# Optimization experiments

Hardware: AMD Instinct MI355X
Metric: run time of the kernel (lower is better)

Reference implementation:

```python
import jax, jax.numpy as jnp
import numpy as np

# Module hyperparameters (from init_kwargs defaults)
SEQ_LEN = 250
MASK_RATIO = 0.6
NUM_SPANS = 3
SPAN_LEN = max(1, int(SEQ_LEN * MASK_RATIO / NUM_SPANS))  # 50
QRS_RADIUS = 30
CENTER = SEQ_LEN // 2  # 125
QRS_START = CENTER - QRS_RADIUS  # 95
QRS_END = CENTER + QRS_RADIUS    # 155
AVOID_PROB = 0.8
MAX_ATTEMPTS = 15


def setup_inputs() -> dict:
    key = jax.random.key(0)
    x = jax.random.normal(key, (16384, 12, SEQ_LEN), dtype=jnp.float32)
    return {"x": x}


def _span_starts(key, B):
    """Vectorized replacement for the host-side rejection-sampling loop.

    For each (batch, span): decide QRS avoidance, draw MAX_ATTEMPTS candidate
    starts at once, take the first valid one, fall back to a fresh draw if all
    attempts overlap the QRS zone (same semantics as the torch retry loop).
    """
    k1, k2, k3 = jax.random.split(key, 3)
    hi = max(1, SEQ_LEN - SPAN_LEN)  # exclusive upper bound = 200
    use_physio = jax.random.uniform(k1, (B, NUM_SPANS)) < AVOID_PROB
    cands = jax.random.randint(k2, (B, NUM_SPANS, MAX_ATTEMPTS), 0, hi)  # (B,S,A)
    ends = jnp.minimum(cands + SPAN_LEN, SEQ_LEN)
    no_overlap = (ends <= QRS_START) | (cands >= QRS_END)
    valid = no_overlap | (~use_physio[..., None])  # (B,S,A)
    first = jnp.argmax(valid, axis=-1)  # first valid attempt index
    chosen = jnp.take_along_axis(cands, first[..., None], axis=-1)[..., 0]
    fallback = jax.random.randint(k3, (B, NUM_SPANS), 0, hi)
    return jnp.where(valid.any(axis=-1), chosen, fallback)  # (B,S)


def reference(x):
    B, C, L = x.shape
    start = _span_starts(jax.random.key(42), B)          # (B, NUM_SPANS)
    end = jnp.minimum(start + SPAN_LEN, L)
    idx = jnp.arange(L)                                   # (L,)
    span_mask = (idx >= start[..., None]) & (idx < end[..., None])  # (B,S,L)
    masks = span_mask.any(axis=1)                         # (B, L) True where masked
    masked_x = x * (~masks)[:, None, :].astype(x.dtype)   # zero masked positions
    return masked_x, masks
```

## Files before the change

### kernel.cpp

```cpp
#include <hip/hip_runtime.h>
#include <stdint.h>

namespace {

constexpr int SEQ    = 250;
constexpr int SPAN   = 50;
constexpr int NSPANS = 3;
constexpr int NATT   = 15;
constexpr int QS     = 95;
constexpr int QE     = 155;
constexpr int NB     = 16384;
constexpr int NCH    = 12;
constexpr uint32_t HI = 200;

struct U2 { uint32_t a, b; };

__host__ __device__ constexpr U2 tf2x32(uint32_t k0, uint32_t k1,
                                        uint32_t x0, uint32_t x1) {
  uint32_t ks[3] = { k0, k1, k0 ^ k1 ^ 0x1BD11BDAu };
  uint32_t rot[2][4] = { {13u, 15u, 26u, 6u}, {17u, 29u, 16u, 24u} };
  x0 += ks[0];
  x1 += ks[1];
  for (int i = 0; i < 5; ++i) {
    for (int j = 0; j < 4; ++j) {
      uint32_t r = rot[i & 1][j];
      x0 += x1;
      x1 = (x1 << r) | (x1 >> (32u - r));
      x1 ^= x0;
    }
    x0 += ks[(i + 1) % 3];
    x1 += ks[(i + 2) % 3] + (uint32_t)(i + 1);
  }
  return U2{x0, x1};
}

constexpr U2 SK1 = tf2x32(0u, 42u, 0u, 0u);
constexpr U2 SK2 = tf2x32(0u, 42u, 0u, 1u);
constexpr U2 SK3 = tf2x32(0u, 42u, 0u, 2u);

constexpr U2 K2H = tf2x32(SK2.a, SK2.b, 0u, 0u);
constexpr U2 K2L = tf2x32(SK2.a, SK2.b, 0u, 1u);
constexpr U2 K3H = tf2x32(SK3.a, SK3.b, 0u, 0u);
constexpr U2 K3L = tf2x32(SK3.a, SK3.b, 0u, 1u);

__device__ __forceinline__ uint32_t rbit(U2 k, uint32_t idx) {
  U2 r = tf2x32(k.a, k.b, 0u, idx);
  return r.a ^ r.b;
}

__device__ __forceinline__ uint32_t draw200(uint32_t h, uint32_t l) {
  return ((h % HI) * 96u + (l % HI)) % HI;
}

__device__ __forceinline__ int compute_start(uint32_t u) {
  uint32_t ub = rbit(SK1, u);
  float uu = __uint_as_float((ub >> 9) | 0x3f800000u) - 1.0f;
  bool physio = (uu < 0.8f);

  for (int a = 0; a < NATT; ++a) {
    uint32_t idx = u * (uint32_t)NATT + (uint32_t)a;
    uint32_t h = rbit(K2H, idx);
    uint32_t l = rbit(K2L, idx);
    int cand = (int)draw200(h, l);
    bool no_ov = (cand + SPAN <= QS) || (cand >= QE);
    if (no_ov || !physio) return cand;
  }
  uint32_t h = rbit(K3H, u);
  uint32_t l = rbit(K3L, u);
  return (int)draw200(h, l);
}

__global__ __launch_bounds__(256)
void k_all(const float4* __restrict__ x4, float4* __restrict__ o4,
           float2* __restrict__ m2) {
  __shared__ int ss[NSPANS];
  const int b = blockIdx.x;
  const int t = threadIdx.x;

  if (t < NSPANS) ss[t] = compute_start((uint32_t)(b * NSPANS + t));
  __syncthreads();
  const int s0 = ss[0], s1 = ss[1], s2 = ss[2];

  const float4* xb = x4 + (size_t)b * (NCH * SEQ / 4);
  float4*       ob = o4 + (size_t)b * (NCH * SEQ / 4);
  for (int i = t; i < NCH * SEQ / 4; i += 256) {
    int pos0 = (i << 2) % SEQ;
    bool mm[4];
    int nmask = 0;
#pragma unroll
    for (int j = 0; j < 4; ++j) {
      int p = pos0 + j;
      if (p >= SEQ) p -= SEQ;
      bool m = ((unsigned)(p - s0) < (unsigned)SPAN) ||
               ((unsigned)(p - s1) < (unsigned)SPAN) ||
               ((unsigned)(p - s2) < (unsigned)SPAN);
      mm[j] = m;
      nmask += (int)m;
    }
    if (nmask == 4) {
      ob[i] = make_float4(0.0f, 0.0f, 0.0f, 0.0f);
    } else {
      float4 v = xb[i];
      if (mm[0]) v.x = 0.0f;
      if (mm[1]) v.y = 0.0f;
      if (mm[2]) v.z = 0.0f;
      if (mm[3]) v.w = 0.0f;
      ob[i] = v;
    }
  }

  if (t < SEQ / 2) {
    int p0 = t * 2;
    bool ma = ((unsigned)(p0 - s0) < (unsigned)SPAN) ||
              ((unsigned)(p0 - s1) < (unsigned)SPAN) ||
              ((unsigned)(p0 - s2) < (unsigned)SPAN);
    int p1 = p0 + 1;
    bool mb = ((unsigned)(p1 - s0) < (unsigned)SPAN) ||
              ((unsigned)(p1 - s1) < (unsigned)SPAN) ||
              ((unsigned)(p1 - s2) < (unsigned)SPAN);
    m2[(size_t)b * (SEQ / 2) + t] = make_float2(ma ? 1.0f : 0.0f,
                                                mb ? 1.0f : 0.0f);
  }
}

}

extern "C" void kernel_launch(void* const* d_in, const int* in_sizes, int n_in,
                              void* d_out, int out_size, void* d_ws, size_t ws_size,
                              hipStream_t stream) {
  const float* x = (const float*)d_in[0];
  float* out = (float*)d_out;
  float* mask_out = out + (size_t)NB * NCH * SEQ;

  k_all<<<NB, 256, 0, stream>>>(
      (const float4*)x, (float4*)out, (float2*)mask_out);
}
```

Before: 336.3 us.

## Parallelize span-start rejection sampling across lanes and use nontemporal memory ops

The serial per-span loop of up to 15 Threefry candidate draws becomes one candidate per lane (45 lanes). A wavefront ballot then picks the first valid attempt per span, with a fallback draw when none is valid. This shortens the serial RNG prologue that every block runs before its streaming work. Loads and stores of x, the output and the mask now use nontemporal builtins to bypass cache retention, and the mask write is moved ahead of the main loop.

New measurement: 323.2 us. 1.04x faster.

```diff
diff --git a/kernel.cpp b/kernel.cpp
--- a/kernel.cpp
+++ b/kernel.cpp
@@ -12,6 +12,9 @@
 constexpr int NB     = 16384;
 constexpr int NCH    = 12;
 constexpr uint32_t HI = 200;
+
+typedef float f32x4 __attribute__((ext_vector_type(4)));
+typedef float f32x2 __attribute__((ext_vector_type(2)));
 
 struct U2 { uint32_t a, b; };
 
@@ -52,37 +55,59 @@
   return ((h % HI) * 96u + (l % HI)) % HI;
 }
 
-__device__ __forceinline__ int compute_start(uint32_t u) {
-  uint32_t ub = rbit(SK1, u);
-  float uu = __uint_as_float((ub >> 9) | 0x3f800000u) - 1.0f;
-  bool physio = (uu < 0.8f);
-
-  for (int a = 0; a < NATT; ++a) {
-    uint32_t idx = u * (uint32_t)NATT + (uint32_t)a;
-    uint32_t h = rbit(K2H, idx);
-    uint32_t l = rbit(K2L, idx);
-    int cand = (int)draw200(h, l);
-    bool no_ov = (cand + SPAN <= QS) || (cand >= QE);
-    if (no_ov || !physio) return cand;
-  }
-  uint32_t h = rbit(K3H, u);
-  uint32_t l = rbit(K3L, u);
-  return (int)draw200(h, l);
-}
-
 __global__ __launch_bounds__(256)
-void k_all(const float4* __restrict__ x4, float4* __restrict__ o4,
-           float2* __restrict__ m2) {
+void k_all(const f32x4* __restrict__ x4, f32x4* __restrict__ o4,
+           f32x2* __restrict__ m2) {
   __shared__ int ss[NSPANS];
   const int b = blockIdx.x;
   const int t = threadIdx.x;
 
-  if (t < NSPANS) ss[t] = compute_start((uint32_t)(b * NSPANS + t));
+  if (t < 64) {
+    const int s = t / NATT;
+    const int a = t - s * NATT;
+    const bool lane_ok = (t < NSPANS * NATT);
+    const uint32_t u = (uint32_t)(b * NSPANS + (lane_ok ? s : 0));
+
+    bool valid = false;
+    int cand = 0;
+    if (lane_ok) {
+      uint32_t ub = rbit(SK1, u);
+      float uu = __uint_as_float((ub >> 9) | 0x3f800000u) - 1.0f;
+      bool physio = (uu < 0.8f);
+      uint32_t idx = u * (uint32_t)NATT + (uint32_t)a;
+      cand = (int)draw200(rbit(K2H, idx), rbit(K2L, idx));
+      bool no_ov = (cand + SPAN <= QS) || (cand >= QE);
+      valid = no_ov || !physio;
+    }
+
+    uint64_t m = __ballot(valid);
+    if (lane_ok) {
+      uint32_t sm = (uint32_t)(m >> (s * NATT)) & 0x7FFFu;
+      bool i_am_first = valid && ((sm & ((1u << a) - 1u)) == 0u);
+      if (i_am_first) ss[s] = cand;
+      if (a == 0 && sm == 0u) {
+        ss[s] = (int)draw200(rbit(K3H, u), rbit(K3L, u));
+      }
+    }
+  }
   __syncthreads();
   const int s0 = ss[0], s1 = ss[1], s2 = ss[2];
 
-  const float4* xb = x4 + (size_t)b * (NCH * SEQ / 4);
-  float4*       ob = o4 + (size_t)b * (NCH * SEQ / 4);
+  if (t < SEQ / 2) {
+    int p0 = t * 2;
+    bool ma = ((unsigned)(p0 - s0) < (unsigned)SPAN) ||
+              ((unsigned)(p0 - s1) < (unsigned)SPAN) ||
+              ((unsigned)(p0 - s2) < (unsigned)SPAN);
+    int p1 = p0 + 1;
+    bool mb = ((unsigned)(p1 - s0) < (unsigned)SPAN) ||
+              ((unsigned)(p1 - s1) < (unsigned)SPAN) ||
+              ((unsigned)(p1 - s2) < (unsigned)SPAN);
+    f32x2 mv = { ma ? 1.0f : 0.0f, mb ? 1.0f : 0.0f };
+    __builtin_nontemporal_store(mv, &m2[(size_t)b * (SEQ / 2) + t]);
+  }
+
+  const f32x4* xb = x4 + (size_t)b * (NCH * SEQ / 4);
+  f32x4*       ob = o4 + (size_t)b * (NCH * SEQ / 4);
   for (int i = t; i < NCH * SEQ / 4; i += 256) {
     int pos0 = (i << 2) % SEQ;
     bool mm[4];
@@ -98,28 +123,16 @@
       nmask += (int)m;
     }
     if (nmask == 4) {
-      ob[i] = make_float4(0.0f, 0.0f, 0.0f, 0.0f);
+      f32x4 z = { 0.0f, 0.0f, 0.0f, 0.0f };
+      __builtin_nontemporal_store(z, &ob[i]);
     } else {
-      float4 v = xb[i];
+      f32x4 v = __builtin_nontemporal_load(&xb[i]);
       if (mm[0]) v.x = 0.0f;
       if (mm[1]) v.y = 0.0f;
       if (mm[2]) v.z = 0.0f;
       if (mm[3]) v.w = 0.0f;
-      ob[i] = v;
+      __builtin_nontemporal_store(v, &ob[i]);
     }
-  }
-
-  if (t < SEQ / 2) {
-    int p0 = t * 2;
-    bool ma = ((unsigned)(p0 - s0) < (unsigned)SPAN) ||
-              ((unsigned)(p0 - s1) < (unsigned)SPAN) ||
-              ((unsigned)(p0 - s2) < (unsigned)SPAN);
-    int p1 = p0 + 1;
-    bool mb = ((unsigned)(p1 - s0) < (unsigned)SPAN) ||
-              ((unsigned)(p1 - s1) < (unsigned)SPAN) ||
-              ((unsigned)(p1 - s2) < (unsigned)SPAN);
-    m2[(size_t)b * (SEQ / 2) + t] = make_float2(ma ? 1.0f : 0.0f,
-                                                mb ? 1.0f : 0.0f);
   }
 }
 
@@ -133,5 +146,5 @@
   float* mask_out = out + (size_t)NB * NCH * SEQ;
 
   k_all<<<NB, 256, 0, stream>>>(
-      (const float4*)x, (float4*)out, (float2*)mask_out);
+      (const f32x4*)x, (f32x4*)out, (f32x2*)mask_out);
 }
```
